# Kernel tuning notes

Measured on AMD Instinct MI355X. Metric: run time of the kernel, lower is better.

## Reference

```python
import jax, jax.numpy as jnp
import numpy as np
import math

S_DIM = 512
Z_DIM = 64
B, L = 64, 512
NUM_HEADS = 4
HEAD_DIM = S_DIM // NUM_HEADS
N_AA = 20


def _layer_norm(x, eps=1e-5):
    mu = jnp.mean(x, axis=-1, keepdims=True)
    var = jnp.var(x, axis=-1, keepdims=True)
    return (x - mu) * jax.lax.rsqrt(var + eps)


def setup_inputs() -> dict:
    key = jax.random.key(0)
    ks = jax.random.split(key, 16)
    scale = 0.02
    d = {
        's': jax.random.normal(ks[0], (B, L, S_DIM), jnp.float32),
        'z': jax.random.normal(ks[1], (B, L, Z_DIM), jnp.float32),
        'wq': jax.random.normal(ks[2], (S_DIM, S_DIM), jnp.float32) * scale,
        'bq': jnp.zeros((S_DIM,), jnp.float32),
        'wk': jax.random.normal(ks[3], (S_DIM, S_DIM), jnp.float32) * scale,
        'bk': jnp.zeros((S_DIM,), jnp.float32),
        'wv': jax.random.normal(ks[4], (S_DIM, S_DIM), jnp.float32) * scale,
        'bv': jnp.zeros((S_DIM,), jnp.float32),
        'wo': jax.random.normal(ks[5], (S_DIM, S_DIM), jnp.float32) * scale,
        'bo': jnp.zeros((S_DIM,), jnp.float32),
        'wp': jax.random.normal(ks[6], (S_DIM, N_AA), jnp.float32) * scale,
        'bp': jnp.zeros((N_AA,), jnp.float32),
        'pos_bias': jax.random.normal(ks[7], (512,), jnp.float32) * 0.3,
        'entropy_weight': jnp.ones((1,), jnp.float32) * 0.1,
        'ln_g': jnp.ones((S_DIM,), jnp.float32),
        'ln_b': jnp.zeros((S_DIM,), jnp.float32),
        'w1': jax.random.normal(ks[8], (S_DIM, 4 * S_DIM), jnp.float32) * scale,
        'b1': jnp.zeros((4 * S_DIM,), jnp.float32),
        'w2': jax.random.normal(ks[9], (4 * S_DIM, S_DIM), jnp.float32) * scale,
        'b2': jnp.zeros((S_DIM,), jnp.float32),
    }
    return d


def reference(s, z, wq, bq, wk, bk, wv, bv, wo, bo, wp, bp, pos_bias,
              entropy_weight, ln_g, ln_b, w1, b1, w2, b2):
    Bc, Lc, D = s.shape
    H, hd = NUM_HEADS, D // NUM_HEADS

    s_ln = _layer_norm(s)  # non-affine F.layer_norm

    # sequence-profile entropy
    logits = s_ln @ wp + bp                      # [B,L,20]
    profile_probs = jax.nn.softmax(logits, axis=-1)
    position_entropy = -jnp.sum(profile_probs * jnp.log(profile_probs + 1e-8), axis=-1)  # [B,L]

    q = (s_ln @ wq + bq).reshape(Bc, Lc, H, hd)
    k = (s_ln @ wk + bk).reshape(Bc, Lc, H, hd)
    v = (s_ln @ wv + bv).reshape(Bc, Lc, H, hd)

    scores = jnp.einsum('blhd,bmhd->bhlm', q, k) / math.sqrt(hd)  # [B,H,L,L]

    # bias injected only at query index 0, using batch-0 entropy (as in torch code)
    entropy_guidance = -position_entropy[0, :Lc] * entropy_weight[0]  # [L]
    total_bias = entropy_guidance + pos_bias[:Lc]                      # [L]
    scores = scores.at[:, :, 0, :].add(total_bias[None, None, :])

    attn_weights = jax.nn.softmax(scores, axis=-1)                     # [B,H,L,L]
    attn_out = jnp.einsum('bhlm,bmhd->blhd', attn_weights, v).reshape(Bc, Lc, D)

    s2 = s + (attn_out @ wo + bo)

    h = _layer_norm(s2) * ln_g + ln_b
    ffn_out = jax.nn.relu(h @ w1 + b1) @ w2 + b2
    s3 = s2 + ffn_out

    return (s3, z, attn_weights[:, 0, :, :], position_entropy, profile_probs)
```

## Files before the change

kernel.cpp:

```cpp
#include <hip/hip_runtime.h>
#include <hip/hip_bf16.h>
#include <math.h>

#define SDIM 512
#define BATCH 64
#define LSEQ 512
#define NHEAD 4
#define HDIM 128
#define NAA 20
#define NROWS (BATCH * LSEQ)
#define LDQKV 1536

typedef __attribute__((ext_vector_type(8))) short short8;
typedef __attribute__((ext_vector_type(4))) float f32x4;

__device__ __forceinline__ unsigned short f2bf(float f) {
    unsigned int x = __float_as_uint(f);
    unsigned int r = (x + 0x7fffu + ((x >> 16) & 1u)) >> 16;
    return (unsigned short)r;
}
__device__ __forceinline__ float bf2f(unsigned short u) {
    return __uint_as_float((unsigned int)u << 16);
}

__device__ __forceinline__ void load16_lds(const void* g, void* lds) {
    __builtin_amdgcn_global_load_lds(
        (const __attribute__((address_space(1))) unsigned int*)g,
        (__attribute__((address_space(3))) unsigned int*)lds, 16, 0, 0);
}

__global__ __launch_bounds__(256) void wtrans(
    const float* __restrict__ W, unsigned short* __restrict__ Wt, int K, int N)
{
    __shared__ float tile[32][33];
    const int t = threadIdx.x, tx = t & 31, ty = t >> 5;
    const int n0 = blockIdx.x * 32, k0 = blockIdx.y * 32;
    #pragma unroll
    for (int p = 0; p < 4; p++)
        tile[ty + p * 8][tx] = W[(size_t)(k0 + ty + p * 8) * N + n0 + tx];
    __syncthreads();
    #pragma unroll
    for (int p = 0; p < 4; p++)
        Wt[(size_t)(n0 + ty + p * 8) * K + k0 + tx] = f2bf(tile[tx][ty + p * 8]);
}

__global__ __launch_bounds__(256) void wptrans(
    const float* __restrict__ wp, unsigned short* __restrict__ wpT)
{
    const int g = blockIdx.x * 256 + threadIdx.x;
    const int k = g & 511, j = g >> 9;
    float v = (j < NAA) ? wp[(size_t)k * NAA + j] : 0.0f;
    wpT[(size_t)j * 512 + k] = f2bf(v);
}

__global__ void bpack(const float* __restrict__ bq, const float* __restrict__ bk,
                      const float* __restrict__ bv, float* __restrict__ bqkv)
{
    int t = threadIdx.x;
    bqkv[t] = bq[t]; bqkv[512 + t] = bk[t]; bqkv[1024 + t] = bv[t];
}

template<int INMODE, bool AFFINE>
__global__ __launch_bounds__(256) void ln_kernel(
    const void* __restrict__ inp, unsigned short* __restrict__ out,
    const float* __restrict__ gamma, const float* __restrict__ beta)
{
    const int w = threadIdx.x >> 6, l = threadIdx.x & 63;
    const int r = blockIdx.x * 4 + w;

    float x[8];
    if (INMODE == 0) {
        const float* row = (const float*)inp + (size_t)r * SDIM;
        float4 a = *(const float4*)(row + l * 4);
        float4 b = *(const float4*)(row + 256 + l * 4);
        x[0] = a.x; x[1] = a.y; x[2] = a.z; x[3] = a.w;
        x[4] = b.x; x[5] = b.y; x[6] = b.z; x[7] = b.w;
    } else {
        const unsigned short* row = (const unsigned short*)inp + (size_t)r * SDIM;
        uint2 a = *(const uint2*)(row + l * 4);
        uint2 b = *(const uint2*)(row + 256 + l * 4);
        x[0] = bf2f((unsigned short)(a.x & 0xffff)); x[1] = bf2f((unsigned short)(a.x >> 16));
        x[2] = bf2f((unsigned short)(a.y & 0xffff)); x[3] = bf2f((unsigned short)(a.y >> 16));
        x[4] = bf2f((unsigned short)(b.x & 0xffff)); x[5] = bf2f((unsigned short)(b.x >> 16));
        x[6] = bf2f((unsigned short)(b.y & 0xffff)); x[7] = bf2f((unsigned short)(b.y >> 16));
    }

    float sum = 0.f, sq = 0.f;
    #pragma unroll
    for (int i = 0; i < 8; i++) { sum += x[i]; sq += x[i] * x[i]; }
    #pragma unroll
    for (int o = 1; o < 64; o <<= 1) {
        sum += __shfl_xor(sum, o);
        sq  += __shfl_xor(sq, o);
    }
    const float mean = sum * (1.0f / SDIM);
    const float var  = sq * (1.0f / SDIM) - mean * mean;
    const float inv  = rsqrtf(var + 1e-5f);

    float y[8];
    if (AFFINE) {
        float4 g0 = *(const float4*)(gamma + l * 4);
        float4 g1 = *(const float4*)(gamma + 256 + l * 4);
        float4 b0 = *(const float4*)(beta + l * 4);
        float4 b1 = *(const float4*)(beta + 256 + l * 4);
        y[0] = (x[0]-mean)*inv*g0.x + b0.x; y[1] = (x[1]-mean)*inv*g0.y + b0.y;
        y[2] = (x[2]-mean)*inv*g0.z + b0.z; y[3] = (x[3]-mean)*inv*g0.w + b0.w;
        y[4] = (x[4]-mean)*inv*g1.x + b1.x; y[5] = (x[5]-mean)*inv*g1.y + b1.y;
        y[6] = (x[6]-mean)*inv*g1.z + b1.z; y[7] = (x[7]-mean)*inv*g1.w + b1.w;
    } else {
        #pragma unroll
        for (int i = 0; i < 8; i++) y[i] = (x[i] - mean) * inv;
    }

    unsigned short* orow = out + (size_t)r * SDIM;
    uint2 p0, p1;
    p0.x = (unsigned)f2bf(y[0]) | ((unsigned)f2bf(y[1]) << 16);
    p0.y = (unsigned)f2bf(y[2]) | ((unsigned)f2bf(y[3]) << 16);
    p1.x = (unsigned)f2bf(y[4]) | ((unsigned)f2bf(y[5]) << 16);
    p1.y = (unsigned)f2bf(y[6]) | ((unsigned)f2bf(y[7]) << 16);
    *(uint2*)(orow + l * 4)       = p0;
    *(uint2*)(orow + 256 + l * 4) = p1;
}

__global__ __launch_bounds__(256) void profile_kernel(
    const unsigned short* __restrict__ A,
    const unsigned short* __restrict__ wpT,
    const float* __restrict__ bp,
    float* __restrict__ probs,
    float* __restrict__ pe)
{
    __shared__ __align__(16) unsigned short As[128 * 64];

    const int t = threadIdx.x;
    const int w = t >> 6, l = t & 63;
    const int lr = l & 15, lg = l >> 4;
    const int m0 = blockIdx.x * 128;

    f32x4 sacc[2][2];
    #pragma unroll
    for (int m = 0; m < 2; m++)
        #pragma unroll
        for (int n = 0; n < 2; n++)
            sacc[m][n] = (f32x4){0.f, 0.f, 0.f, 0.f};

    const int srow  = l >> 3;
    const int swz16 = ((l & 7) ^ srow) << 4;
    const char* pA[4];
    unsigned ldsoff[4];
    #pragma unroll
    for (int i = 0; i < 4; i++) {
        const int row = (w * 4 + i) * 8 + srow;
        pA[i] = (const char*)A + (size_t)(m0 + row) * 1024 + swz16;
        ldsoff[i] = (unsigned)(w * 4 + i) * 1024;
    }

    const int rsw   = (lr & 7) << 4;
    const int foff0 = (lg * 16) ^ rsw;
    const int foff1 = (64 + lg * 16) ^ rsw;
    int arow[2];
    #pragma unroll
    for (int m = 0; m < 2; m++) arow[m] = (w * 32 + m * 16 + lr) * 128;

    for (int k0 = 0; k0 < 512; k0 += 64) {
        const size_t kb = (size_t)k0 * 2;
        #pragma unroll
        for (int i = 0; i < 4; i++)
            load16_lds(pA[i] + kb, (char*)As + ldsoff[i]);
        __syncthreads();

        short8 af[2], bf[2];
        #pragma unroll
        for (int m = 0; m < 2; m++) af[m] = *(const short8*)((const char*)As + arow[m] + foff0);
        #pragma unroll
        for (int n = 0; n < 2; n++)
            bf[n] = *(const short8*)(wpT + (size_t)(n * 16 + lr) * 512 + k0 + lg * 8);
        #pragma unroll
        for (int m = 0; m < 2; m++)
            #pragma unroll
            for (int n = 0; n < 2; n++)
                sacc[m][n] = __builtin_amdgcn_mfma_f32_16x16x32_bf16(af[m], bf[n], sacc[m][n], 0, 0, 0);

        #pragma unroll
        for (int m = 0; m < 2; m++) af[m] = *(const short8*)((const char*)As + arow[m] + foff1);
        #pragma unroll
        for (int n = 0; n < 2; n++)
            bf[n] = *(const short8*)(wpT + (size_t)(n * 16 + lr) * 512 + k0 + 32 + lg * 8);
        #pragma unroll
        for (int m = 0; m < 2; m++)
            #pragma unroll
            for (int n = 0; n < 2; n++)
                sacc[m][n] = __builtin_amdgcn_mfma_f32_16x16x32_bf16(af[m], bf[n], sacc[m][n], 0, 0, 0);

        __syncthreads();
    }

    const float b0 = bp[lr];
    const float b1 = (lr < 4) ? bp[16 + lr] : 0.0f;
    #pragma unroll
    for (int m = 0; m < 2; m++) {
        #pragma unroll
        for (int j = 0; j < 4; j++) {
            const float v0 = sacc[m][0][j] + b0;
            const float e0 = __expf(v0);
            const float v1 = sacc[m][1][j] + b1;
            const float e1 = (lr < 4) ? __expf(v1) : 0.0f;
            float Sp = e0 + e1;
            float Tp = e0 * v0 + ((lr < 4) ? e1 * v1 : 0.0f);
            #pragma unroll
            for (int o = 1; o < 16; o <<= 1) {
                Sp += __shfl_xor(Sp, o);
                Tp += __shfl_xor(Tp, o);
            }
            const float inv = 1.0f / Sp;
            const int row = m0 + w * 32 + m * 16 + lg * 4 + j;
            probs[(size_t)row * NAA + lr] = e0 * inv;
            if (lr < 4) probs[(size_t)row * NAA + 16 + lr] = e1 * inv;
            if (lr == 0) pe[row] = logf(Sp) - Tp * inv;
        }
    }
}

__global__ void bias_kernel(const float* __restrict__ pe,
                            const float* __restrict__ ew,
                            const float* __restrict__ pos,
                            float* __restrict__ tb)
{
    int t = threadIdx.x;
    tb[t] = -pe[t] * ew[0] + pos[t];
}

template<int OMODE, bool BIAS, bool RELU, int RESID>
__global__ __launch_bounds__(256, 3) void mgemm3(
    const unsigned short* __restrict__ A, int lda,
    const unsigned short* __restrict__ Bt, int ldb,
    void* __restrict__ Cv, int ldc,
    const float* __restrict__ bias,
    const void* __restrict__ R, int ldr,
    int K)
{
    __shared__ __align__(16) char lds[49152];

    const int t = threadIdx.x;
    const int w = t >> 6, l = t & 63;
    const int wr = w >> 1, wc = w & 1;
    const int lg = l >> 4, lr = l & 15;

    const int gx   = gridDim.x;
    const int nwg  = gx * gridDim.y;
    const int flat = blockIdx.x + gx * blockIdx.y;
    const int cpx  = nwg >> 3;
    const int logical = (flat & 7) * cpx + (flat >> 3);
    const int m0 = (logical / gx) * 128, n0 = (logical % gx) * 128;

    f32x4 acc[4][4];
    #pragma unroll
    for (int m = 0; m < 4; m++)
        #pragma unroll
        for (int n = 0; n < 4; n++)
            acc[m][n] = (f32x4){0.f, 0.f, 0.f, 0.f};

    const char* srcA[2];
    const char* srcB[2];
    #pragma unroll
    for (int j = 0; j < 2; j++) {
        const int s   = j * 256 + t;
        const int r2  = s >> 3, cc = s & 7;
        const int ccs = cc ^ (r2 & 7);
        const int grow = r2 * 2 + (ccs >> 2);
        const int gch  = ccs & 3;
        srcA[j] = (const char*)A  + ((size_t)(m0 + grow) * lda + gch * 8) * 2;
        srcB[j] = (const char*)Bt + ((size_t)(n0 + grow) * ldb + gch * 8) * 2;
    }

    const int nt = K >> 5;

    auto stage = [&](int kt, int bb) {
        char* db = (char*)lds + bb;
        const size_t kb = (size_t)kt * 64;
        #pragma unroll
        for (int j = 0; j < 2; j++) {
            load16_lds(srcA[j] + kb, db + j * 4096 + t * 16);
            load16_lds(srcB[j] + kb, db + 8192 + j * 4096 + t * 16);
        }
    };

    stage(0, 0);
    stage(1, 16384);

    int b0 = 0, b1 = 16384, b2 = 32768;

    const int laneoff = (lr >> 1) * 128 + (((((lr & 1) << 2) | lg) ^ (lr >> 1)) << 4);

    for (int kt = 0; kt < nt; ++kt) {
        if (kt + 1 < nt) { asm volatile("s_waitcnt vmcnt(4)" ::: "memory"); }
        else             { asm volatile("s_waitcnt vmcnt(0)" ::: "memory"); }
        __builtin_amdgcn_s_barrier();
        asm volatile("" ::: "memory");

        if (kt + 2 < nt) stage(kt + 2, b2);

        const char* Ab = (const char*)lds + b0;
        const char* Bb = Ab + 8192;

        short8 af[4], bf[4];
        #pragma unroll
        for (int m = 0; m < 4; m++)
            af[m] = *(const short8*)(Ab + wr * 4096 + m * 1024 + laneoff);
        #pragma unroll
        for (int n = 0; n < 4; n++)
            bf[n] = *(const short8*)(Bb + wc * 4096 + n * 1024 + laneoff);

        __builtin_amdgcn_s_setprio(1);
        #pragma unroll
        for (int m = 0; m < 4; m++)
            #pragma unroll
            for (int n = 0; n < 4; n++)
                acc[m][n] = __builtin_amdgcn_mfma_f32_16x16x32_bf16(af[m], bf[n], acc[m][n], 0, 0, 0);
        __builtin_amdgcn_s_setprio(0);
        asm volatile("" ::: "memory");

        const int tmp = b0; b0 = b1; b1 = b2; b2 = tmp;
    }

    #pragma unroll
    for (int n = 0; n < 4; n++) {
        const int col = n0 + wc * 64 + n * 16 + lr;
        const float bv = BIAS ? bias[col] : 0.0f;
        #pragma unroll
        for (int m = 0; m < 4; m++) {
            const int rb = m0 + wr * 64 + m * 16 + lg * 4;
            #pragma unroll
            for (int j = 0; j < 4; j++) {
                float v = acc[m][n][j] + bv;
                if (RELU) v = fmaxf(v, 0.f);
                const size_t row = (size_t)(rb + j);
                if (RESID == 1) v += ((const float*)R)[row * ldr + col];
                if (RESID == 2) v += bf2f(((const unsigned short*)R)[row * ldr + col]);
                if (OMODE == 0) {
                    ((float*)Cv)[row * ldc + col] = v;
                } else {
                    ((unsigned short*)Cv)[row * ldc + col] = f2bf(v);
                }
            }
        }
    }
}

__global__ __launch_bounds__(256, 3) void attn_mfma(
    const unsigned short* __restrict__ QKV,
    const float* __restrict__ tb,
    unsigned short* __restrict__ AOb,
    float* __restrict__ lgout)
{
    const int flat = blockIdx.x + 4 * (blockIdx.y + 4 * blockIdx.z);
    const int logical = ((flat & 7) << 7) + (flat >> 3);
    const int qt = logical & 3;
    const int h  = (logical >> 2) & 3;
    const int b  = logical >> 4;
    const int t  = threadIdx.x;
    const int w  = t >> 6, l = t & 63;
    const int lr = l & 15, lg = l >> 4;
    const int qbase = qt * 128 + w * 32;

    const unsigned short* Qp = QKV;
    const unsigned short* Kp = QKV + 512;
    const unsigned short* Vp = QKV + 1024;

    __shared__ __align__(16) unsigned short Ks[64 * 128];
    __shared__ __align__(16) unsigned short Vt[128 * 64];
    __shared__ __align__(16) unsigned short Pl[4 * 2048];
    __shared__ float tbs[512];

    tbs[t] = tb[t];
    tbs[t + 256] = tb[t + 256];

    short8 qf[2][4];
    #pragma unroll
    for (int fc = 0; fc < 2; fc++) {
        const size_t qrow = (size_t)(b * LSEQ + qbase + fc * 16 + lr) * LDQKV + h * HDIM;
        #pragma unroll
        for (int ks = 0; ks < 4; ks++)
            qf[fc][ks] = *(const short8*)(Qp + qrow + ks * 32 + lg * 8);
    }

    f32x4 oacc[2][8];
    #pragma unroll
    for (int m = 0; m < 2; m++)
        #pragma unroll
        for (int n = 0; n < 8; n++)
            oacc[m][n] = (f32x4){0.f, 0.f, 0.f, 0.f};
    float lpart[2] = {0.f, 0.f};

    const float scale = 0.08838834764831845f;
    unsigned short* Plw = Pl + w * 2048;

    for (int kt = 0; kt < 8; ++kt) {
        __syncthreads();

        const int k0 = (l & 31) * 2;
        const int d0 = w * 32 + (l >> 5) * 16;
        const size_t vrow = (size_t)(b * LSEQ + kt * 64 + k0) * LDQKV + h * HDIM + d0;
        short8 va0 = *(const short8*)(Vp + vrow);
        short8 va1 = *(const short8*)(Vp + vrow + 8);
        short8 vb0 = *(const short8*)(Vp + vrow + LDQKV);
        short8 vb1 = *(const short8*)(Vp + vrow + LDQKV + 8);

        #pragma unroll
        for (int it = 0; it < 4; it++) {
            const int bi = it * 4 + w;
            const int r  = bi * 4 + lg;
            const int sc = lr ^ (r & 7);
            const char* src = (const char*)Kp +
                (size_t)(b * LSEQ + kt * 64 + r) * (LDQKV * 2) + h * 256 + sc * 16;
            load16_lds(src, (char*)Ks + bi * 1024);
        }

        #pragma unroll
        for (int j = 0; j < 16; j++) {
            const int d = d0 + j;
            unsigned short lo = (unsigned short)((j < 8) ? va0[j] : va1[j - 8]);
            unsigned short hi = (unsigned short)((j < 8) ? vb0[j] : vb1[j - 8]);
            unsigned int pk = (unsigned)lo | ((unsigned)hi << 16);
            const int addr = d * 128 + ((((k0 >> 3) ^ (d & 7))) << 4) + (k0 & 7) * 2;
            *(unsigned int*)((char*)Vt + addr) = pk;
        }
        __syncthreads();

        f32x4 sacc[4][2];
        #pragma unroll
        for (int fm = 0; fm < 4; fm++)
            #pragma unroll
            for (int fc = 0; fc < 2; fc++)
                sacc[fm][fc] = (f32x4){0.f, 0.f, 0.f, 0.f};
        #pragma unroll
        for (int ks = 0; ks < 4; ks++) {
            short8 af[4];
            #pragma unroll
            for (int fm = 0; fm < 4; fm++) {
                const int r2 = fm * 16 + lr;
                af[fm] = *(const short8*)((const char*)Ks +
                          r2 * 256 + (((ks * 4 + lg) ^ (lr & 7)) << 4));
            }
            #pragma unroll
            for (int fm = 0; fm < 4; fm++)
                #pragma unroll
                for (int fc = 0; fc < 2; fc++)
                    sacc[fm][fc] = __builtin_amdgcn_mfma_f32_16x16x32_bf16(
                        af[fm], qf[fc][ks], sacc[fm][fc], 0, 0, 0);
        }

        #pragma unroll
        for (int fm = 0; fm < 4; fm++) {
            #pragma unroll
            for (int fc = 0; fc < 2; fc++) {
                float p0 = sacc[fm][fc][0] * scale;
                float p1 = sacc[fm][fc][1] * scale;
                float p2 = sacc[fm][fc][2] * scale;
                float p3 = sacc[fm][fc][3] * scale;
                if (qt == 0 && w == 0 && fc == 0 && lr == 0) {
                    const int kb = kt * 64 + fm * 16 + lg * 4;
                    p0 += tbs[kb + 0]; p1 += tbs[kb + 1];
                    p2 += tbs[kb + 2]; p3 += tbs[kb + 3];
                }
                p0 = __expf(p0); p1 = __expf(p1);
                p2 = __expf(p2); p3 = __expf(p3);
                lpart[fc] += (p0 + p1) + (p2 + p3);
                const int rq = fc * 16 + lr;
                const int chunk = fm * 2 + (lg >> 1);
                const int addr = rq * 128 + ((chunk ^ (rq & 7)) << 4) + (lg & 1) * 8;
                unsigned int lo = (unsigned)f2bf(p0) | ((unsigned)f2bf(p1) << 16);
                unsigned int hi = (unsigned)f2bf(p2) | ((unsigned)f2bf(p3) << 16);
                *(uint2*)((char*)Plw + addr) = make_uint2(lo, hi);
            }
        }

        #pragma unroll
        for (int ks2 = 0; ks2 < 2; ks2++) {
            short8 pf[2];
            #pragma unroll
            for (int fm2 = 0; fm2 < 2; fm2++) {
                const int rq2 = fm2 * 16 + lr;
                pf[fm2] = *(const short8*)((const char*)Plw +
                           rq2 * 128 + (((ks2 * 4 + lg) ^ (rq2 & 7)) << 4));
            }
            #pragma unroll
            for (int fn = 0; fn < 8; fn++) {
                const int d = fn * 16 + lr;
                short8 vf = *(const short8*)((const char*)Vt +
                             d * 128 + (((ks2 * 4 + lg) ^ (d & 7)) << 4));
                #pragma unroll
                for (int fm2 = 0; fm2 < 2; fm2++)
                    oacc[fm2][fn] = __builtin_amdgcn_mfma_f32_16x16x32_bf16(
                        pf[fm2], vf, oacc[fm2][fn], 0, 0, 0);
            }
        }
    }

    float l0 = lpart[0], l1 = lpart[1];
    l0 += __shfl_xor(l0, 16); l0 += __shfl_xor(l0, 32);
    l1 += __shfl_xor(l1, 16); l1 += __shfl_xor(l1, 32);
    float* lw = (float*)Plw;
    if (lg == 0) { lw[lr] = l0; lw[16 + lr] = l1; }
    if (h == 0 && lg == 0) {
        lgout[b * LSEQ + qbase + lr]      = l0;
        lgout[b * LSEQ + qbase + 16 + lr] = l1;
    }
    __builtin_amdgcn_s_waitcnt(0);

    #pragma unroll
    for (int fm2 = 0; fm2 < 2; fm2++) {
        float linv[4];
        #pragma unroll
        for (int j = 0; j < 4; j++)
            linv[j] = 1.0f / lw[fm2 * 16 + lg * 4 + j];
        #pragma unroll
        for (int fn = 0; fn < 8; fn++) {
            const int d = fn * 16 + lr;
            #pragma unroll
            for (int j = 0; j < 4; j++) {
                const int q = qbase + fm2 * 16 + lg * 4 + j;
                AOb[(size_t)(b * LSEQ + q) * SDIM + h * HDIM + d] =
                    f2bf(oacc[fm2][fn][j] * linv[j]);
            }
        }
    }
}

__global__ __launch_bounds__(256) void sw0_kernel(
    const unsigned short* __restrict__ QKV,
    const float* __restrict__ tb,
    const float* __restrict__ lsum,
    float* __restrict__ W0)
{
    const int flat = blockIdx.x + 4 * blockIdx.y;
    const int logical = ((flat & 7) << 5) + (flat >> 3);
    const int qt = logical & 3;
    const int b  = logical >> 2;
    const int t  = threadIdx.x;
    const int w  = t >> 6, l = t & 63;
    const int lr = l & 15, lg = l >> 4;
    const int qbase = qt * 128 + w * 32;

    const unsigned short* Qp = QKV;
    const unsigned short* Kp = QKV + 512;

    __shared__ __align__(16) unsigned short Ks[64 * 128];
    __shared__ __align__(16) float Sc[4][32][68];

    short8 qf[2][4];
    #pragma unroll
    for (int fc = 0; fc < 2; fc++) {
        const size_t qrow = (size_t)(b * LSEQ + qbase + fc * 16 + lr) * LDQKV;
        #pragma unroll
        for (int ks = 0; ks < 4; ks++)
            qf[fc][ks] = *(const short8*)(Qp + qrow + ks * 32 + lg * 8);
    }

    float linv[2];
    linv[0] = 1.0f / lsum[b * LSEQ + qbase + lr];
    linv[1] = 1.0f / lsum[b * LSEQ + qbase + 16 + lr];

    const float scale = 0.08838834764831845f;

    for (int kt = 0; kt < 8; ++kt) {
        __syncthreads();
        #pragma unroll
        for (int it = 0; it < 4; it++) {
            const int bi = it * 4 + w;
            const int r  = bi * 4 + lg;
            const int sc = lr ^ (r & 7);
            const char* src = (const char*)Kp +
                (size_t)(b * LSEQ + kt * 64 + r) * (LDQKV * 2) + sc * 16;
            load16_lds(src, (char*)Ks + bi * 1024);
        }
        __syncthreads();

        f32x4 sacc[4][2];
        #pragma unroll
        for (int fm = 0; fm < 4; fm++)
            #pragma unroll
            for (int fc = 0; fc < 2; fc++)
                sacc[fm][fc] = (f32x4){0.f, 0.f, 0.f, 0.f};
        #pragma unroll
        for (int ks = 0; ks < 4; ks++) {
            short8 af[4];
            #pragma unroll
            for (int fm = 0; fm < 4; fm++) {
                const int r2 = fm * 16 + lr;
                af[fm] = *(const short8*)((const char*)Ks +
                          r2 * 256 + (((ks * 4 + lg) ^ (lr & 7)) << 4));
            }
            #pragma unroll
            for (int fm = 0; fm < 4; fm++)
                #pragma unroll
                for (int fc = 0; fc < 2; fc++)
                    sacc[fm][fc] = __builtin_amdgcn_mfma_f32_16x16x32_bf16(
                        af[fm], qf[fc][ks], sacc[fm][fc], 0, 0, 0);
        }

        #pragma unroll
        for (int fm = 0; fm < 4; fm++) {
            #pragma unroll
            for (int fc = 0; fc < 2; fc++) {
                float p0 = sacc[fm][fc][0] * scale;
                float p1 = sacc[fm][fc][1] * scale;
                float p2 = sacc[fm][fc][2] * scale;
                float p3 = sacc[fm][fc][3] * scale;
                if (qt == 0 && w == 0 && fc == 0 && lr == 0) {
                    const int kb = kt * 64 + fm * 16 + lg * 4;
                    p0 += tb[kb + 0]; p1 += tb[kb + 1];
                    p2 += tb[kb + 2]; p3 += tb[kb + 3];
                }
                p0 = __expf(p0) * linv[fc]; p1 = __expf(p1) * linv[fc];
                p2 = __expf(p2) * linv[fc]; p3 = __expf(p3) * linv[fc];
                *(float4*)&Sc[w][fc * 16 + lr][fm * 16 + lg * 4] =
                    make_float4(p0, p1, p2, p3);
            }
        }

        #pragma unroll
        for (int i = 0; i < 8; i++) {
            const int row = i * 4 + lg;
            float4 v = *(const float4*)&Sc[w][row][lr * 4];
            *(float4*)(W0 + (size_t)(b * LSEQ + qbase + row) * LSEQ +
                       kt * 64 + lr * 4) = v;
        }
    }
}

extern "C" void kernel_launch(void* const* d_in, const int* in_sizes, int n_in,
                              void* d_out, int out_size, void* d_ws, size_t ws_size,
                              hipStream_t stream)
{
    const float* s   = (const float*)d_in[0];
    const float* z   = (const float*)d_in[1];
    const float* wq  = (const float*)d_in[2];
    const float* bq  = (const float*)d_in[3];
    const float* wk  = (const float*)d_in[4];
    const float* bk  = (const float*)d_in[5];
    const float* wv  = (const float*)d_in[6];
    const float* bv  = (const float*)d_in[7];
    const float* wo  = (const float*)d_in[8];
    const float* bo  = (const float*)d_in[9];
    const float* wp  = (const float*)d_in[10];
    const float* bp  = (const float*)d_in[11];
    const float* pos = (const float*)d_in[12];
    const float* ew  = (const float*)d_in[13];
    const float* lng = (const float*)d_in[14];
    const float* lnb = (const float*)d_in[15];
    const float* w1  = (const float*)d_in[16];
    const float* b1  = (const float*)d_in[17];
    const float* w2  = (const float*)d_in[18];
    const float* b2  = (const float*)d_in[19];

    float* out = (float*)d_out;
    const size_t oz  = (size_t)NROWS * SDIM;
    const size_t ow  = oz + (size_t)NROWS * 64;
    const size_t ope = ow + (size_t)NROWS * LSEQ;
    const size_t opr = ope + (size_t)NROWS;

    char* wsb = (char*)d_ws;
    unsigned short* QKV = (unsigned short*)(wsb);
    unsigned short* F   = (unsigned short*)(wsb);
    unsigned short* Xb  = (unsigned short*)(wsb + 100663296);
    unsigned short* s2b = (unsigned short*)(wsb + 134217728);
    unsigned short* hb  = (unsigned short*)(wsb + 167772160);
    unsigned short* wqkvt = (unsigned short*)(wsb + 234881024);
    unsigned short* wot = wqkvt + 786432;
    unsigned short* w1t = wqkvt + 1048576;
    unsigned short* w2t = wqkvt + 2097152;
    unsigned short* wpT = wqkvt + 3145728;
    float* bqkv = (float*)(wsb + 234881024 + 6324224);
    float* tb   = bqkv + 1536;
    float* lgv  = tb + 512;

    wtrans<<<dim3(16, 16), 256, 0, stream>>>(wq, wqkvt, 512, 512);
    wtrans<<<dim3(16, 16), 256, 0, stream>>>(wk, wqkvt + 262144, 512, 512);
    wtrans<<<dim3(16, 16), 256, 0, stream>>>(wv, wqkvt + 524288, 512, 512);
    wtrans<<<dim3(16, 16), 256, 0, stream>>>(wo, wot, 512, 512);
    wtrans<<<dim3(64, 16), 256, 0, stream>>>(w1, w1t, 512, 2048);
    wtrans<<<dim3(16, 64), 256, 0, stream>>>(w2, w2t, 2048, 512);
    wptrans<<<64, 256, 0, stream>>>(wp, wpT);
    bpack<<<1, 512, 0, stream>>>(bq, bk, bv, bqkv);

    ln_kernel<0, false><<<NROWS / 4, 256, 0, stream>>>(s, Xb, nullptr, nullptr);

    profile_kernel<<<256, 256, 0, stream>>>(Xb, wpT, bp, out + opr, out + ope);

    bias_kernel<<<1, 512, 0, stream>>>(out + ope, ew, pos, tb);

    mgemm3<1, true, false, 0><<<dim3(12, 256), 256, 0, stream>>>(
        Xb, 512, wqkvt, 512, QKV, LDQKV, bqkv, nullptr, 0, 512);

    attn_mfma<<<dim3(4, NHEAD, BATCH), 256, 0, stream>>>(
        QKV, tb, Xb, lgv);

    sw0_kernel<<<dim3(4, BATCH), 256, 0, stream>>>(QKV, tb, lgv, out + ow);

    mgemm3<1, true, false, 1><<<dim3(4, 256), 256, 0, stream>>>(
        Xb, 512, wot, 512, s2b, 512, bo, s, 512, 512);

    ln_kernel<1, true><<<NROWS / 4, 256, 0, stream>>>(s2b, hb, lng, lnb);

    mgemm3<1, true, true, 0><<<dim3(16, 256), 256, 0, stream>>>(
        hb, 512, w1t, 512, F, 2048, b1, nullptr, 0, 512);

    mgemm3<0, true, false, 2><<<dim3(4, 256), 256, 0, stream>>>(
        F, 2048, w2t, 2048, out, 512, b2, s2b, 512, 2048);

    hipMemcpyAsync(out + oz, z, (size_t)NROWS * 64 * sizeof(float),
                   hipMemcpyDeviceToDevice, stream);
}
```

Before: 484.3 us.

## Enlarge GEMM tiles to 256x256 with 512 threads and BK=64 double buffering

Replaces the 128x128, 256-thread GEMM with a 256x256 tile computed by 8 waves, each holding a 128x64 accumulator. The K step grows to 64, with a new swizzled LDS layout and a two-buffer pipeline in place of the three-buffer one. The goal is more data reuse per global load and fewer workgroups. In exchange it uses 128KB of LDS and many more accumulator registers, lowers occupancy, and adds a second barrier per K iteration. The FFN2 and out-projection GEMMs now launch only 256 workgroups.

```diff
diff --git a/kernel.cpp b/kernel.cpp
--- a/kernel.cpp
+++ b/kernel.cpp
@@ -230,7 +230,7 @@
 }
 
 template<int OMODE, bool BIAS, bool RELU, int RESID>
-__global__ __launch_bounds__(256, 3) void mgemm3(
+__global__ __launch_bounds__(512, 2) void mgemm4(
     const unsigned short* __restrict__ A, int lda,
     const unsigned short* __restrict__ Bt, int ldb,
     void* __restrict__ Cv, int ldc,
@@ -238,11 +238,11 @@
     const void* __restrict__ R, int ldr,
     int K)
 {
-    __shared__ __align__(16) char lds[49152];
+    __shared__ __align__(16) char lds[131072];
 
     const int t = threadIdx.x;
     const int w = t >> 6, l = t & 63;
-    const int wr = w >> 1, wc = w & 1;
+    const int wr = w >> 2, wc = w & 3;
     const int lg = l >> 4, lr = l & 15;
 
     const int gx   = gridDim.x;
@@ -250,76 +250,72 @@
     const int flat = blockIdx.x + gx * blockIdx.y;
     const int cpx  = nwg >> 3;
     const int logical = (flat & 7) * cpx + (flat >> 3);
-    const int m0 = (logical / gx) * 128, n0 = (logical % gx) * 128;
-
-    f32x4 acc[4][4];
-    #pragma unroll
-    for (int m = 0; m < 4; m++)
+    const int m0 = (logical / gx) * 256, n0 = (logical % gx) * 256;
+
+    f32x4 acc[8][4];
+    #pragma unroll
+    for (int m = 0; m < 8; m++)
         #pragma unroll
         for (int n = 0; n < 4; n++)
             acc[m][n] = (f32x4){0.f, 0.f, 0.f, 0.f};
 
-    const char* srcA[2];
-    const char* srcB[2];
-    #pragma unroll
-    for (int j = 0; j < 2; j++) {
-        const int s   = j * 256 + t;
-        const int r2  = s >> 3, cc = s & 7;
-        const int ccs = cc ^ (r2 & 7);
-        const int grow = r2 * 2 + (ccs >> 2);
-        const int gch  = ccs & 3;
-        srcA[j] = (const char*)A  + ((size_t)(m0 + grow) * lda + gch * 8) * 2;
-        srcB[j] = (const char*)Bt + ((size_t)(n0 + grow) * ldb + gch * 8) * 2;
-    }
-
-    const int nt = K >> 5;
+    const int srow = l >> 3;
+    const int scol = (l & 7) ^ srow;
+    const char* pA = (const char*)A  + ((size_t)(m0 + srow) * lda + scol * 8) * 2;
+    const char* pB = (const char*)Bt + ((size_t)(n0 + srow) * ldb + scol * 8) * 2;
+    const size_t ldab = (size_t)lda * 16;
+    const size_t ldbb = (size_t)ldb * 16;
+
+    const int nt = K >> 6;
 
     auto stage = [&](int kt, int bb) {
         char* db = (char*)lds + bb;
-        const size_t kb = (size_t)kt * 64;
-        #pragma unroll
-        for (int j = 0; j < 2; j++) {
-            load16_lds(srcA[j] + kb, db + j * 4096 + t * 16);
-            load16_lds(srcB[j] + kb, db + 8192 + j * 4096 + t * 16);
-        }
+        const size_t kb = (size_t)kt * 128;
+        #pragma unroll
+        for (int u = 0; u < 4; u++)
+            load16_lds(pA + (size_t)(u * 8 + w) * ldab + kb, db + (u * 8 + w) * 1024);
+        #pragma unroll
+        for (int u = 0; u < 4; u++)
+            load16_lds(pB + (size_t)(u * 8 + w) * ldbb + kb, db + 32768 + (u * 8 + w) * 1024);
     };
 
     stage(0, 0);
-    stage(1, 16384);
-
-    int b0 = 0, b1 = 16384, b2 = 32768;
-
-    const int laneoff = (lr >> 1) * 128 + (((((lr & 1) << 2) | lg) ^ (lr >> 1)) << 4);
+    stage(1, 65536);
 
     for (int kt = 0; kt < nt; ++kt) {
-        if (kt + 1 < nt) { asm volatile("s_waitcnt vmcnt(4)" ::: "memory"); }
+        if (kt + 1 < nt) { asm volatile("s_waitcnt vmcnt(8)" ::: "memory"); }
         else             { asm volatile("s_waitcnt vmcnt(0)" ::: "memory"); }
         __builtin_amdgcn_s_barrier();
         asm volatile("" ::: "memory");
 
-        if (kt + 2 < nt) stage(kt + 2, b2);
-
-        const char* Ab = (const char*)lds + b0;
-        const char* Bb = Ab + 8192;
-
-        short8 af[4], bf[4];
-        #pragma unroll
-        for (int m = 0; m < 4; m++)
-            af[m] = *(const short8*)(Ab + wr * 4096 + m * 1024 + laneoff);
-        #pragma unroll
-        for (int n = 0; n < 4; n++)
-            bf[n] = *(const short8*)(Bb + wc * 4096 + n * 1024 + laneoff);
-
-        __builtin_amdgcn_s_setprio(1);
-        #pragma unroll
-        for (int m = 0; m < 4; m++)
+        const char* Ab = (const char*)lds + (kt & 1) * 65536;
+        const char* Bb = Ab + 32768;
+
+        #pragma unroll
+        for (int ks = 0; ks < 2; ks++) {
+            const int csw = ((ks * 4 + lg) ^ (lr & 7)) << 4;
+            short8 af[8], bf[4];
+            #pragma unroll
+            for (int m = 0; m < 8; m++)
+                af[m] = *(const short8*)(Ab + (wr * 128 + m * 16 + lr) * 128 + csw);
             #pragma unroll
             for (int n = 0; n < 4; n++)
-                acc[m][n] = __builtin_amdgcn_mfma_f32_16x16x32_bf16(af[m], bf[n], acc[m][n], 0, 0, 0);
-        __builtin_amdgcn_s_setprio(0);
+                bf[n] = *(const short8*)(Bb + (wc * 64 + n * 16 + lr) * 128 + csw);
+
+            __builtin_amdgcn_s_setprio(1);
+            #pragma unroll
+            for (int m = 0; m < 8; m++)
+                #pragma unroll
+                for (int n = 0; n < 4; n++)
+                    acc[m][n] = __builtin_amdgcn_mfma_f32_16x16x32_bf16(
+                        af[m], bf[n], acc[m][n], 0, 0, 0);
+            __builtin_amdgcn_s_setprio(0);
+        }
+
         asm volatile("" ::: "memory");
-
-        const int tmp = b0; b0 = b1; b1 = b2; b2 = tmp;
+        __builtin_amdgcn_s_barrier();
+        asm volatile("" ::: "memory");
+        if (kt + 2 < nt) stage(kt + 2, (kt & 1) * 65536);
     }
 
     #pragma unroll
@@ -327,8 +323,8 @@
         const int col = n0 + wc * 64 + n * 16 + lr;
         const float bv = BIAS ? bias[col] : 0.0f;
         #pragma unroll
-        for (int m = 0; m < 4; m++) {
-            const int rb = m0 + wr * 64 + m * 16 + lg * 4;
+        for (int m = 0; m < 8; m++) {
+            const int rb = m0 + wr * 128 + m * 16 + lg * 4;
             #pragma unroll
             for (int j = 0; j < 4; j++) {
                 float v = acc[m][n][j] + bv;
@@ -689,7 +685,7 @@
 
     bias_kernel<<<1, 512, 0, stream>>>(out + ope, ew, pos, tb);
 
-    mgemm3<1, true, false, 0><<<dim3(12, 256), 256, 0, stream>>>(
+    mgemm4<1, true, false, 0><<<dim3(6, 128), 512, 0, stream>>>(
         Xb, 512, wqkvt, 512, QKV, LDQKV, bqkv, nullptr, 0, 512);
 
     attn_mfma<<<dim3(4, NHEAD, BATCH), 256, 0, stream>>>(
@@ -697,15 +693,15 @@
 
     sw0_kernel<<<dim3(4, BATCH), 256, 0, stream>>>(QKV, tb, lgv, out + ow);
 
-    mgemm3<1, true, false, 1><<<dim3(4, 256), 256, 0, stream>>>(
+    mgemm4<1, true, false, 1><<<dim3(2, 128), 512, 0, stream>>>(
         Xb, 512, wot, 512, s2b, 512, bo, s, 512, 512);
 
     ln_kernel<1, true><<<NROWS / 4, 256, 0, stream>>>(s2b, hb, lng, lnb);
 
-    mgemm3<1, true, true, 0><<<dim3(16, 256), 256, 0, stream>>>(
+    mgemm4<1, true, true, 0><<<dim3(8, 128), 512, 0, stream>>>(
         hb, 512, w1t, 512, F, 2048, b1, nullptr, 0, 512);
 
-    mgemm3<0, true, false, 2><<<dim3(4, 256), 256, 0, stream>>>(
+    mgemm4<0, true, false, 2><<<dim3(2, 128), 512, 0, stream>>>(
         F, 2048, w2t, 2048, out, 512, b2, s2b, 512, 2048);
 
     hipMemcpyAsync(out + oz, z, (size_t)NROWS * 64 * sizeof(float),
```

Measured after the change: 508.3 us. 5.0% more time.
